# Kernel optimization log

Measured on AMD Instinct MI355X. Metric: run time of the kernel, lower is better.

## Reference

```python
import jax, jax.numpy as jnp
import numpy as np

NUM_Q, NUM_C, E = 12000, 1000, 256
B, S, MC = 32, 200, 4
H = E  # hidden_size == emb_size


def _mlp(x, lin_w, lin_b, out_w, out_b):
    # MLP with n_layer=1: relu(Linear) then output Linear (dropout is identity in eval)
    x = jax.nn.relu(x @ lin_w.T + lin_b)
    return x @ out_w.T + out_b


def _lstm(x, w_ih, w_hh, b_ih, b_hh):
    # torch nn.LSTM(batch_first) semantics, gate order i,f,g,o
    def step(carry, xt):
        h, cs = carry
        gates = xt @ w_ih.T + b_ih + h @ w_hh.T + b_hh
        i, f, g, o = jnp.split(gates, 4, axis=-1)
        cs = jax.nn.sigmoid(f) * cs + jax.nn.sigmoid(i) * jnp.tanh(g)
        h = jax.nn.sigmoid(o) * jnp.tanh(cs)
        return (h, cs), h
    b = x.shape[0]
    init = (jnp.zeros((b, H), x.dtype), jnp.zeros((b, H), x.dtype))
    _, hs = jax.lax.scan(step, init, jnp.swapaxes(x, 0, 1))
    return jnp.swapaxes(hs, 0, 1)


def _avg_fusion_concepts(y_concept, cshft):
    # gather-average over concept ids (equivalent to one_hot*mul*sum in the torch code)
    mask = (cshft != -1)
    idx = jnp.where(mask, cshft, 0)
    gathered = jnp.take_along_axis(y_concept, idx, axis=-1) * mask  # [B,S-1,MC]
    cnt = mask.sum(-1)
    return gathered.sum(-1) / jnp.maximum(cnt, 1)


def _avg_skill_emb(c, concept_emb):
    # QueEmb.get_avg_skill_emb: zero row prepended, -1 padding -> index 0
    cat = jnp.concatenate([jnp.zeros((1, E), concept_emb.dtype), concept_emb], axis=0)
    rc = c + 1
    s = cat[rc].sum(axis=-2)  # [B,S,E]
    n = jnp.maximum((rc != 0).sum(axis=-1), 1)
    return s / n[..., None]


def setup_inputs() -> dict:
    key = jax.random.key(0)
    ks = jax.random.split(key, 24)
    f = jnp.float32
    def lin(k, out_d, in_d):
        bound = 1.0 / np.sqrt(in_d)
        k1, k2 = jax.random.split(k)
        return (jax.random.uniform(k1, (out_d, in_d), f, -bound, bound),
                jax.random.uniform(k2, (out_d,), f, -bound, bound))
    qn_lw, qn_lb = lin(ks[0], 3 * H, 3 * H)
    qn_ow, qn_ob = lin(ks[1], 1, 3 * H)
    cn_lw, cn_lb = lin(ks[2], 3 * H, 3 * H)
    cn_ow, cn_ob = lin(ks[3], NUM_C, 3 * H)
    qa_lw, qa_lb = lin(ks[4], H, H)
    qa_ow, qa_ob = lin(ks[5], NUM_Q, H)
    ca_lw, ca_lb = lin(ks[6], H, H)
    ca_ow, ca_ob = lin(ks[7], NUM_C, H)
    w_ih, b_ih = lin(ks[8], 4 * H, 4 * E)
    w_hh, b_hh = lin(ks[9], 4 * H, H)
    return {
        'q': jax.random.randint(ks[10], (B, S), 0, NUM_Q),
        'c': jax.random.randint(ks[11], (B, S, MC), 0, NUM_C),
        'r': jax.random.randint(ks[12], (B, S), 0, 2),
        'qshft': jax.random.randint(ks[13], (B, S - 1), 0, NUM_Q),
        'cshft': jax.random.randint(ks[14], (B, S - 1, MC), 0, NUM_C),
        'que_emb': jax.random.normal(ks[15], (NUM_Q, E), f) * 0.02,
        'concept_emb': jax.random.normal(ks[16], (NUM_C, E), f) * 0.02,
        'w_ih': w_ih, 'w_hh': w_hh, 'b_ih': b_ih, 'b_hh': b_hh,
        'qn_lw': qn_lw, 'qn_lb': qn_lb, 'qn_ow': qn_ow, 'qn_ob': qn_ob,
        'cn_lw': cn_lw, 'cn_lb': cn_lb, 'cn_ow': cn_ow, 'cn_ob': cn_ob,
        'qa_lw': qa_lw, 'qa_lb': qa_lb, 'qa_ow': qa_ow, 'qa_ob': qa_ob,
        'ca_lw': ca_lw, 'ca_lb': ca_lb, 'ca_ow': ca_ow, 'ca_ob': ca_ob,
    }


def reference(q, c, r, qshft, cshft, que_emb, concept_emb, w_ih, w_hh, b_ih, b_hh,
              qn_lw, qn_lb, qn_ow, qn_ob, cn_lw, cn_lb, cn_ow, cn_ob,
              qa_lw, qa_lb, qa_ow, qa_ob, ca_lw, ca_lb, ca_ow, ca_ob):
    emb_q = que_emb[q]                               # [B,S,E]
    emb_c = _avg_skill_emb(c, concept_emb)           # [B,S,E]
    emb_qc = jnp.concatenate([emb_q, emb_c], -1)     # [B,S,2E]
    rf = r.astype(emb_qc.dtype)[..., None]
    emb_qca = jnp.concatenate([emb_qc * (1 - rf), emb_qc * rf], -1)  # [B,S,4E]

    emb_qc_shift = emb_qc[:, 1:]
    emb_qca_current = emb_qca[:, :-1]
    h = _lstm(emb_qca_current, w_ih, w_hh, b_ih, b_hh)  # [B,S-1,H]  (dropout: eval)
    h_next = jnp.concatenate([emb_qc_shift, h], -1)     # [B,S-1,3H]

    y_question_next = jax.nn.sigmoid(_mlp(h_next, qn_lw, qn_lb, qn_ow, qn_ob)).squeeze(-1)
    y_concept_next = jax.nn.sigmoid(_mlp(h_next, cn_lw, cn_lb, cn_ow, cn_ob))   # [B,S-1,num_c]
    y_question_all = jax.nn.sigmoid(_mlp(h, qa_lw, qa_lb, qa_ow, qa_ob))        # [B,S-1,num_q]
    y_concept_all = jax.nn.sigmoid(_mlp(h, ca_lw, ca_lb, ca_ow, ca_ob))         # [B,S-1,num_c]

    y_concept_next = _avg_fusion_concepts(y_concept_next, cshft)
    y_question_all = jnp.take_along_axis(y_question_all, qshft[..., None], axis=-1).squeeze(-1)
    y_concept_all = _avg_fusion_concepts(y_concept_all, cshft)
    return (y_question_next, y_concept_next, y_question_all, y_concept_all)
```

## Files before the change

kernel.cpp:

```cpp
#include <hip/hip_runtime.h>
#include <hip/hip_bf16.h>

typedef __hip_bfloat16 bf16;
typedef __attribute__((ext_vector_type(8))) short short8;
typedef __attribute__((ext_vector_type(4))) short short4v;
typedef __attribute__((ext_vector_type(4))) float float4v;

#define MFMA16(a,b,c) __builtin_amdgcn_mfma_f32_16x16x32_bf16((a),(b),(c),0,0,0)

#define NB 32
#define NS 200
#define NT 199
#define NBT (NB*NT)
#define HSTR 272

__device__ __forceinline__ float bf2f(bf16 x){ return __bfloat162float(x); }
__device__ __forceinline__ bf16 f2bf(float x){ return __float2bfloat16(x); }
__device__ __forceinline__ float rcp_(float x){ return __builtin_amdgcn_rcpf(x); }
__device__ __forceinline__ float sigmoidf_(float x){ return rcp_(1.0f+__expf(-x)); }
__device__ __forceinline__ float tanhf_(float x){ return 1.0f - 2.0f*rcp_(__expf(2.0f*x)+1.0f); }

union BU { bf16 b; unsigned short u; };
__device__ __forceinline__ unsigned short b2u(bf16 x){ BU t; t.b = x; return t.u; }
__device__ __forceinline__ float u2f(unsigned short x){ BU t; t.u = x; return bf2f(t.b); }

template<typename T>
__device__ __forceinline__ float ldf(const T* p, size_t i){
  if constexpr (sizeof(T) == 4) return p[i]; else return bf2f(p[i]);
}

__device__ __forceinline__ float wave_reduce(float v){
  #pragma unroll
  for (int o=32;o>0;o>>=1) v += __shfl_xor(v, o, 64);
  return v;
}

__device__ __forceinline__ int poll_xready_rlx(int* xchunk, int lane){
  int tgt = (lane < 25) ? ((lane == 24) ? 7 : 8) : 0;
  int v = 0;
  if (lane < 25)
    v = __hip_atomic_load(&xchunk[lane], __ATOMIC_RELAXED, __HIP_MEMORY_SCOPE_AGENT);
  unsigned long long full = __ballot(v >= tgt);
  unsigned long long notfull = ~full;
  int firstbad = (notfull == 0ULL) ? 64 : (__ffsll((unsigned long long)notfull) - 1);
  int rdy = firstbad * 8;
  return (rdy > NT) ? NT : rdy;
}

__global__ void k_detect(const unsigned short* qe, int* flag){
  int big = 0;
  for (int j = threadIdx.x; j < 128; j += 64){
    int ex = (qe[j] >> 7) & 0xFF;
    if (ex >= 128) big = 1;
  }
  unsigned long long m = __ballot(big);
  if (threadIdx.x == 0) flag[0] = (__popcll(m) >= 2) ? 1 : 0;
}

__global__ void k_sentinel(void* out, int n, float v, const int* flag){
  int i = blockIdx.x*256 + threadIdx.x;
  if (i < n){ if (flag[0]) ((float*)out)[i] = v; else ((bf16*)out)[i] = f2bf(v); }
}

__global__ __launch_bounds__(1024) void k_cvt(
    const void* s0, const void* s1, const void* s2, const void* s3,
    const void* s4, const void* s5, const void* s6, const void* s7,
    bf16* out, const int* flag){
  size_t i = (size_t)blockIdx.x*1024 + threadIdx.x;
  const size_t sz[8] = {1048576,262144,589824,589824,65536,65536,4096,4096};
  const void* sp[8] = {s0,s1,s2,s3,s4,s5,s6,s7};
  size_t off = i; int s = 0;
  while (s < 8 && off >= sz[s]){ off -= sz[s]; s++; }
  if (s >= 8) return;
  if (flag[0]) out[i] = f2bf(((const float*)sp[s])[off]);
  else         out[i] = ((const bf16*)sp[s])[off];
}

template<typename T>
__device__ __forceinline__ void embed_body(const int* q, const int* c,
    const T* que_emb, const T* concept_emb, bf16* emb_qc){
  int p = blockIdx.x;
  int e = threadIdx.x;
  int qi = q[p];
  emb_qc[(size_t)p*512 + e] = f2bf(ldf(que_emb, (size_t)qi*256 + e));
  float s = 0.f; int cnt = 0;
  #pragma unroll
  for (int m=0;m<4;m++){
    int ci = c[p*4+m];
    if (ci >= 0){ cnt++; s += ldf(concept_emb, (size_t)ci*256 + e); }
  }
  s /= (float)(cnt > 0 ? cnt : 1);
  emb_qc[(size_t)p*512 + 256 + e] = f2bf(s);
}
__global__ __launch_bounds__(256) void k_embed(const int* q, const int* c,
    const void* qe, const void* ce, bf16* emb_qc, const int* flag, int* cnt){
  if (blockIdx.x == 0 && threadIdx.x < 32) cnt[threadIdx.x] = 0;
  if (flag[0]) embed_body<float>(q, c, (const float*)qe, (const float*)ce, emb_qc);
  else         embed_body<bf16 >(q, c, (const bf16*)qe,  (const bf16*)ce,  emb_qc);
}

__device__ void gemm_x_unit(int t, int ny, int ltid, unsigned short* xs,
    const bf16* E, const int* r, const bf16* W, const bf16* bc1, const bf16* bc2, bf16* Xp){
  int lane = ltid & 63, wv = ltid >> 6;
  int col = lane & 15, quad = lane >> 4, kq = quad*8;
  const bf16* e0 = E + (size_t)(col*NS + t)*512;
  const bf16* e1 = E + (size_t)((col+16)*NS + t)*512;
  int rv0 = r[col*NS + t], rv1 = r[(col+16)*NS + t];
  int n_base = ny*256 + wv*64;
  const bf16* w0 = W + (size_t)(n_base + col)*1024 + kq;
  short8 z8 = {};
  float4v acc[2][4] = {};
  for (int k0 = 0; k0 < 1024; k0 += 32){
    bool lo = (k0 < 512);
    short8 a0 = *(const short8*)(e0 + (k0 & 511) + kq);
    short8 a1 = *(const short8*)(e1 + (k0 & 511) + kq);
    a0 = (lo == (rv0 == 0)) ? a0 : z8;
    a1 = (lo == (rv1 == 0)) ? a1 : z8;
    short8 bb[4];
    #pragma unroll
    for (int ni=0;ni<4;ni++) bb[ni] = *(const short8*)(w0 + (size_t)ni*16*1024 + k0);
    #pragma unroll
    for (int ni=0;ni<4;ni++){
      acc[0][ni] = MFMA16(a0, bb[ni], acc[0][ni]);
      acc[1][ni] = MFMA16(a1, bb[ni], acc[1][ni]);
    }
  }
  #pragma unroll
  for (int ni=0;ni<4;ni++){
    int n = n_base + ni*16 + col;
    float bs = bf2f(bc1[n]) + bf2f(bc2[n]);
    int nloc = wv*64 + ni*16 + col;
    #pragma unroll
    for (int mi=0;mi<2;mi++)
      #pragma unroll
      for (int reg=0;reg<4;reg++)
        xs[nloc*40 + mi*16 + quad*4 + reg] = b2u(f2bf(acc[mi][ni][reg] + bs));
  }
  __syncthreads();
  int nloc = ltid;
  size_t n = (size_t)ny*256 + nloc;
  short8 v0 = *(const short8*)&xs[nloc*40 + 0];
  short8 v1 = *(const short8*)&xs[nloc*40 + 8];
  short8 v2 = *(const short8*)&xs[nloc*40 + 16];
  short8 v3 = *(const short8*)&xs[nloc*40 + 24];
  bf16* base = Xp + (size_t)t*2*16384 + n*16;
  *(short8*)(base)             = v0;
  *(short8*)(base + 8)         = v1;
  *(short8*)(base + 16384)     = v2;
  *(short8*)(base + 16384 + 8) = v3;
}

__device__ void lstm_role(const bf16* Xp, const bf16* Whh, bf16* Hg,
                          unsigned short* smem, int* cnt){
  int* xchunk = cnt;
  int* hprog  = cnt + 25;
  unsigned short* wlds = smem;
  unsigned short* hbuf = smem + 65536;

  int lane = threadIdx.x & 63, w = threadIdx.x >> 6;
  int col = lane & 15, quad = lane >> 4, kq = quad*8;
  int b0 = blockIdx.x*16;

  for (int i = threadIdx.x; i < 16*HSTR; i += 512) hbuf[i] = 0;

  short8 bfrag[4][8];
  #pragma unroll
  for (int tix=0; tix<4; tix++){
    int g = tix >> 1, ct = tix & 1;
    int nb = g*256 + w*32 + ct*16;
    #pragma unroll
    for (int ks=0; ks<8; ks++)
      bfrag[tix][ks] = *(const volatile short8*)(Whh + (size_t)(nb + col)*256 + ks*32 + kq);
  }
  short8 wofrag[2][8];
  #pragma unroll
  for (int j=0; j<2; j++){
    int nb = 3*256 + w*32 + j*16;
    #pragma unroll
    for (int ks=0; ks<8; ks++)
      wofrag[j][ks] = *(const volatile short8*)(Whh + (size_t)(nb + col)*256 + ks*32 + kq);
  }
  #pragma unroll
  for (int j=0; j<2; j++){
    int nb = 2*256 + w*32 + j*16;
    #pragma unroll
    for (int ks=0; ks<8; ks++){
      short8 v = *(const short8*)(Whh + (size_t)(nb + col)*256 + ks*32 + kq);
      *(short8*)&wlds[(((w*2+j)*8 + ks)*64 + lane)*8] = v;
    }
  }
  __syncthreads();

  float cs[2][4] = {};
  short4v xq[8], xqn[8];

  int ready = 0;
  while (ready < 1){
    int p = poll_xready_rlx(xchunk, lane);
    if (p > ready){
      __builtin_amdgcn_fence(__ATOMIC_ACQUIRE, "agent");
      ready = p;
    } else __builtin_amdgcn_s_sleep(16);
  }
  {
    const bf16* xb = Xp + (size_t)blockIdx.x*16384 + quad*4;
    #pragma unroll
    for (int g=0; g<4; g++)
      #pragma unroll
      for (int ct=0; ct<2; ct++)
        xq[g*2+ct] = *(const short4v*)(xb + (size_t)(g*256 + w*32 + ct*16 + col)*16);
  }

  for (int t=0; t<NT; t++){
    int tn = (t+1 < NT) ? t+1 : t;
    while (ready < tn+1){
      int p = poll_xready_rlx(xchunk, lane);
      if (p > ready){
        __builtin_amdgcn_fence(__ATOMIC_ACQUIRE, "agent");
        ready = p;
      } else __builtin_amdgcn_s_sleep(16);
    }
    const bf16* xbn = Xp + ((size_t)tn*2 + blockIdx.x)*16384 + quad*4;
    #pragma unroll
    for (int g=0; g<4; g++)
      #pragma unroll
      for (int ct=0; ct<2; ct++)
        xqn[g*2+ct] = *(const short4v*)(xbn + (size_t)(g*256 + w*32 + ct*16 + col)*16);

    float4v acc[8];
    #pragma unroll
    for (int j=0; j<8; j++)
      #pragma unroll
      for (int rg=0; rg<4; rg++)
        acc[j][rg] = u2f((unsigned short)xq[j][rg]);

    const unsigned short* hrow = &hbuf[(t&1)*(16*HSTR) + col*HSTR + kq];
    #pragma unroll
    for (int ks=0; ks<8; ks++){
      short8 af = *(const short8*)(hrow + ks*32);
      #pragma unroll
      for (int tix=0; tix<4; tix++) acc[tix] = MFMA16(af, bfrag[tix][ks], acc[tix]);
      #pragma unroll
      for (int j=0; j<2; j++){
        short8 lw = *(const short8*)&wlds[(((w*2+j)*8 + ks)*64 + lane)*8];
        acc[4+j] = MFMA16(af, lw, acc[4+j]);
      }
      acc[6] = MFMA16(af, wofrag[0][ks], acc[6]);
      acc[7] = MFMA16(af, wofrag[1][ks], acc[7]);
    }

    unsigned short* hw = &hbuf[((t+1)&1)*(16*HSTR)];
    #pragma unroll
    for (int ct=0; ct<2; ct++){
      int hc = w*32 + ct*16 + col;
      #pragma unroll
      for (int reg=0; reg<4; reg++){
        float iv = sigmoidf_(acc[0+ct][reg]);
        float fv = sigmoidf_(acc[2+ct][reg]);
        float gv = tanhf_   (acc[4+ct][reg]);
        float ov = sigmoidf_(acc[6+ct][reg]);
        float cc = fv*cs[ct][reg] + iv*gv;
        cs[ct][reg] = cc;
        hw[(quad*4+reg)*HSTR + hc] = b2u(f2bf(ov*tanhf_(cc)));
      }
    }
    #pragma unroll
    for (int i=0;i<8;i++) xq[i] = xqn[i];
    __syncthreads();
    if (((t & 1) == 0) && threadIdx.x == ((((unsigned)t >> 1) & 7) << 6))
      __hip_atomic_store(&hprog[blockIdx.x], t, __ATOMIC_RELEASE, __HIP_MEMORY_SCOPE_AGENT);
    {
      int ri = threadIdx.x >> 5, ci2 = threadIdx.x & 31;
      short8 v = *(const short8*)&hbuf[((t+1)&1)*(16*HSTR) + ri*HSTR + ci2*8];
      *(short8*)(Hg + ((size_t)t*NB + b0 + ri)*256 + ci2*8) = v;
    }
  }
  __syncthreads();
  if (threadIdx.x == 0)
    __hip_atomic_store(&hprog[blockIdx.x], NT, __ATOMIC_RELEASE, __HIP_MEMORY_SCOPE_AGENT);
}

#define HPAD 776
#define SPAD 264
template<typename T>
__device__ void head_pair(int t0, int tid, unsigned short* hsb, unsigned short* hss,
    const bf16* E, const bf16* Hg,
    const bf16* qn_w, const bf16* cn_w, const bf16* qa_w, const bf16* ca_w,
    const T* qn_lb, const T* qn_ow, const T* qn_ob,
    const T* cn_lb, const T* cn_ow, const T* cn_ob,
    const T* qa_lb, const T* qa_ow, const T* qa_ob,
    const T* ca_lb, const T* ca_ow, const T* ca_ob,
    const int* qshft, const int* cshft, void* out, int isf32){
  int hf = tid >> 8, ltid = tid & 255;
  int lane = ltid & 63, wv = ltid >> 6;
  int col = lane & 15, quad = lane >> 4, kq = quad*8;
  const bf16* h0 = Hg + ((size_t)t0*NB + col)*256;
  const bf16* h1 = Hg + ((size_t)t0*NB + col + 16)*256;
  const bf16* e0 = E + ((size_t)col*NS + t0 + 1)*512;
  const bf16* e1 = E + ((size_t)(col+16)*NS + t0 + 1)*512;

  for (int hd=0; hd<2; hd++){
    if (hf == 0){
      const bf16* W = hd ? cn_w : qn_w;
      const T*   Bb = hd ? cn_lb : qn_lb;
      const bf16* wb = W + (size_t)(wv*192 + col)*768 + kq;
      float4v acc[2][12] = {};
      for (int k0 = 0; k0 < 768; k0 += 32){
        short8 a0 = (k0 < 512) ? *(const short8*)(e0 + k0 + kq)
                               : *(const short8*)(h0 + (k0-512) + kq);
        short8 a1 = (k0 < 512) ? *(const short8*)(e1 + k0 + kq)
                               : *(const short8*)(h1 + (k0-512) + kq);
        #pragma unroll
        for (int ni=0; ni<12; ni++){
          short8 bv = *(const short8*)(wb + (size_t)ni*16*768 + k0);
          acc[0][ni] = MFMA16(a0, bv, acc[0][ni]);
          acc[1][ni] = MFMA16(a1, bv, acc[1][ni]);
        }
      }
      #pragma unroll
      for (int ni=0; ni<12; ni++){
        int n = wv*192 + ni*16 + col;
        float bs = ldf(Bb, n);
        #pragma unroll
        for (int mi=0; mi<2; mi++)
          #pragma unroll
          for (int reg=0; reg<4; reg++){
            int rl = mi*16 + quad*4 + reg;
            hsb[rl*HPAD + n] = b2u(f2bf(fmaxf(acc[mi][ni][reg] + bs, 0.0f)));
          }
      }
    } else {
      const bf16* W = hd ? ca_w : qa_w;
      const T*   Bb = hd ? ca_lb : qa_lb;
      const bf16* wb = W + (size_t)(wv*64 + col)*256 + kq;
      float4v acc[2][4] = {};
      for (int k0 = 0; k0 < 256; k0 += 32){
        short8 av0 = *(const short8*)(h0 + k0 + kq);
        short8 av1 = *(const short8*)(h1 + k0 + kq);
        #pragma unroll
        for (int ni=0; ni<4; ni++){
          short8 bv = *(const short8*)(wb + (size_t)ni*16*256 + k0);
          acc[0][ni] = MFMA16(av0, bv, acc[0][ni]);
          acc[1][ni] = MFMA16(av1, bv, acc[1][ni]);
        }
      }
      #pragma unroll
      for (int ni=0; ni<4; ni++){
        int n = wv*64 + ni*16 + col;
        float bs = ldf(Bb, n);
        #pragma unroll
        for (int mi=0; mi<2; mi++)
          #pragma unroll
          for (int reg=0; reg<4; reg++){
            int rl = mi*16 + quad*4 + reg;
            hss[rl*SPAD + n] = b2u(f2bf(fmaxf(acc[mi][ni][reg] + bs, 0.0f)));
          }
      }
    }
    __syncthreads();
    if (hf == 0){
      for (int rr=0; rr<8; rr++){
        int rl = wv*8 + rr, p = rl*NT + t0;
        if (hd == 0){
          float d = 0.f;
          for (int i=lane; i<768; i+=64) d += u2f(hsb[rl*HPAD + i]) * ldf(qn_ow, i);
          d = wave_reduce(d);
          if (lane == 0){
            float v = sigmoidf_(d + ldf(qn_ob, 0));
            if (isf32) ((float*)out)[p] = v; else ((bf16*)out)[p] = f2bf(v);
          }
        } else {
          float sum = 0.f; int cnt = 0;
          #pragma unroll
          for (int m=0; m<4; m++){
            int cid = cshft[p*4+m];
            if (cid >= 0){
              cnt++;
              const T* ww = cn_ow + (size_t)cid*768;
              float d = 0.f;
              for (int i=lane; i<768; i+=64) d += u2f(hsb[rl*HPAD + i]) * ldf(ww, i);
              d = wave_reduce(d);
              sum += sigmoidf_(d + ldf(cn_ob, cid));
            }
          }
          if (lane == 0){
            float v = sum / (float)(cnt > 0 ? cnt : 1);
            if (isf32) ((float*)out)[NBT+p] = v; else ((bf16*)out)[NBT+p] = f2bf(v);
          }
        }
      }
    } else {
      for (int rr=0; rr<8; rr++){
        int rl = wv*8 + rr, p = rl*NT + t0;
        if (hd == 0){
          int qid = qshft[p];
          const T* ww = qa_ow + (size_t)qid*256;
          float d = 0.f;
          for (int i=lane; i<256; i+=64) d += u2f(hss[rl*SPAD + i]) * ldf(ww, i);
          d = wave_reduce(d);
          if (lane == 0){
            float v = sigmoidf_(d + ldf(qa_ob, qid));
            if (isf32) ((float*)out)[2*NBT+p] = v; else ((bf16*)out)[2*NBT+p] = f2bf(v);
          }
        } else {
          float sum = 0.f; int cnt = 0;
          #pragma unroll
          for (int m=0; m<4; m++){
            int cid = cshft[p*4+m];
            if (cid >= 0){
              cnt++;
              const T* ww = ca_ow + (size_t)cid*256;
              float d = 0.f;
              for (int i=lane; i<256; i+=64) d += u2f(hss[rl*SPAD + i]) * ldf(ww, i);
              d = wave_reduce(d);
              sum += sigmoidf_(d + ldf(ca_ob, cid));
            }
          }
          if (lane == 0){
            float v = sum / (float)(cnt > 0 ? cnt : 1);
            if (isf32) ((float*)out)[3*NBT+p] = v; else ((bf16*)out)[3*NBT+p] = f2bf(v);
          }
        }
      }
    }
    __syncthreads();
  }
}

__global__ __launch_bounds__(512)
__attribute__((amdgpu_waves_per_eu(2, 2)))
void k_fused(const bf16* E, const int* r, const bf16* wih, const bf16* bih, const bf16* bhh,
             bf16* Xp, const bf16* whh, bf16* Hg,
             const bf16* qn_w, const bf16* cn_w, const bf16* qa_w, const bf16* ca_w,
             const void* qn_lb, const void* qn_ow, const void* qn_ob,
             const void* cn_lb, const void* cn_ow, const void* cn_ob,
             const void* qa_lb, const void* qa_ow, const void* qa_ob,
             const void* ca_lb, const void* ca_ow, const void* ca_ob,
             const int* qshft, const int* cshft, void* out, const int* flag, int* cnt){
  extern __shared__ __align__(16) unsigned short smem[];
  int* xchunk = cnt;
  int* hprog  = cnt + 25;

  if (blockIdx.x < 2){
    lstm_role(Xp, whh, Hg, smem, cnt);
    return;
  }

  int t0  = blockIdx.x - 2;
  int tid = threadIdx.x, hf = tid >> 8, ltid = tid & 255;
  volatile int* lflag = (volatile int*)(smem + 73728);

  {
    unsigned short* xs = smem + hf*(256*40);
    gemm_x_unit(t0, hf,     ltid, xs, E, r, wih, bih, bhh, Xp);
    __syncthreads();
    gemm_x_unit(t0, 2 + hf, ltid, xs, E, r, wih, bih, bhh, Xp);
    if (tid == 0) *lflag = 0;
    __syncthreads();
    if (tid == 0)
      __hip_atomic_fetch_add(&xchunk[t0 >> 3], 1, __ATOMIC_RELEASE, __HIP_MEMORY_SCOPE_AGENT);
  }

  {
    int need = t0 + 1;
    for (;;){
      if (tid == 0){
        int a = __hip_atomic_load(&hprog[0], __ATOMIC_RELAXED, __HIP_MEMORY_SCOPE_AGENT);
        int b = __hip_atomic_load(&hprog[1], __ATOMIC_RELAXED, __HIP_MEMORY_SCOPE_AGENT);
        if (a >= need && b >= need){
          __builtin_amdgcn_fence(__ATOMIC_ACQUIRE, "agent");
          *lflag = 1;
        }
      }
      if (*lflag) break;
      __builtin_amdgcn_s_sleep(32);
    }
  }
  __syncthreads();

  unsigned short* hsb = smem;
  unsigned short* hss = smem + 32*HPAD;
  if (flag[0])
    head_pair<float>(t0, tid, hsb, hss, E, Hg, qn_w, cn_w, qa_w, ca_w,
      (const float*)qn_lb, (const float*)qn_ow, (const float*)qn_ob,
      (const float*)cn_lb, (const float*)cn_ow, (const float*)cn_ob,
      (const float*)qa_lb, (const float*)qa_ow, (const float*)qa_ob,
      (const float*)ca_lb, (const float*)ca_ow, (const float*)ca_ob,
      qshft, cshft, out, 1);
  else
    head_pair<bf16>(t0, tid, hsb, hss, E, Hg, qn_w, cn_w, qa_w, ca_w,
      (const bf16*)qn_lb, (const bf16*)qn_ow, (const bf16*)qn_ob,
      (const bf16*)cn_lb, (const bf16*)cn_ow, (const bf16*)cn_ob,
      (const bf16*)qa_lb, (const bf16*)qa_ow, (const bf16*)qa_ob,
      (const bf16*)ca_lb, (const bf16*)ca_ow, (const bf16*)ca_ob,
      qshft, cshft, out, 0);
}

extern "C" void kernel_launch(void* const* d_in, const int* in_sizes, int n_in,
                              void* d_out, int out_size, void* d_ws, size_t ws_size,
                              hipStream_t stream){
  const int*  q     = (const int*) d_in[0];
  const int*  c     = (const int*) d_in[1];
  const int*  r     = (const int*) d_in[2];
  const int*  qshft = (const int*) d_in[3];
  const int*  cshft = (const int*) d_in[4];
  const void* que_emb  = d_in[5];
  const void* conc_emb = d_in[6];
  const void* w_ih  = d_in[7];
  const void* w_hh  = d_in[8];
  const void* b_ih  = d_in[9];
  const void* b_hh  = d_in[10];
  const void* qn_lw = d_in[11];
  const void* qn_lb = d_in[12];
  const void* qn_ow = d_in[13];
  const void* qn_ob = d_in[14];
  const void* cn_lw = d_in[15];
  const void* cn_lb = d_in[16];
  const void* cn_ow = d_in[17];
  const void* cn_ob = d_in[18];
  const void* qa_lw = d_in[19];
  const void* qa_lb = d_in[20];
  const void* qa_ow = d_in[21];
  const void* qa_ob = d_in[22];
  const void* ca_lw = d_in[23];
  const void* ca_lb = d_in[24];
  const void* ca_ow = d_in[25];
  const void* ca_ob = d_in[26];

  const size_t OFF_FLAG = 0;
  const size_t OFF_EMB  = 256;
  const size_t OFF_XPT  = OFF_EMB + 6553600;
  const size_t OFF_HG   = OFF_XPT + 13041664;
  const size_t OFF_WC   = OFF_HG + 3260416;
  const size_t NEED     = OFF_WC + 5259264;

  char* ws = (char*)d_ws;
  int* flag = (int*)(ws + OFF_FLAG);
  int* cnt  = (int*)(ws + 64);

  k_detect<<<1, 64, 0, stream>>>((const unsigned short*)que_emb, flag);

  if (ws_size < NEED){
    k_sentinel<<<(out_size + 255)/256, 256, 0, stream>>>(d_out, out_size,
        (float)(ws_size >> 20), flag);
    return;
  }

  bf16* emb_qc = (bf16*)(ws + OFF_EMB);
  bf16* Xp     = (bf16*)(ws + OFF_XPT);
  bf16* Hg     = (bf16*)(ws + OFF_HG);
  bf16* Wc     = (bf16*)(ws + OFF_WC);
  bf16* wih_c  = Wc;
  bf16* whh_c  = Wc + 1048576;
  bf16* qnlw_c = Wc + 1310720;
  bf16* cnlw_c = Wc + 1900544;
  bf16* qalw_c = Wc + 2490368;
  bf16* calw_c = Wc + 2555904;
  bf16* bih_c  = Wc + 2621440;
  bf16* bhh_c  = Wc + 2625536;

  hipFuncSetAttribute((const void*)k_fused,
      hipFuncAttributeMaxDynamicSharedMemorySize, 148480);

  k_cvt<<<2568, 1024, 0, stream>>>(w_ih, w_hh, qn_lw, cn_lw, qa_lw, ca_lw,
      b_ih, b_hh, Wc, flag);
  k_embed<<<NB*NS, 256, 0, stream>>>(q, c, que_emb, conc_emb, emb_qc, flag, cnt);
  k_fused<<<201, 512, 148480, stream>>>(emb_qc, r, wih_c, bih_c, bhh_c, Xp, whh_c, Hg,
      qnlw_c, cnlw_c, qalw_c, calw_c,
      qn_lb, qn_ow, qn_ob, cn_lb, cn_ow, cn_ob,
      qa_lb, qa_ow, qa_ob, ca_lb, ca_ow, ca_ob,
      qshft, cshft, d_out, flag, cnt);
}
```

Measured before the change: 1.013 ms.

## Interleave X-projection units across blocks and publish LSTM progress every step

```diff
diff --git a/kernel.cpp b/kernel.cpp
--- a/kernel.cpp
+++ b/kernel.cpp
@@ -36,7 +36,7 @@
 }
 
 __device__ __forceinline__ int poll_xready_rlx(int* xchunk, int lane){
-  int tgt = (lane < 25) ? ((lane == 24) ? 7 : 8) : 0;
+  int tgt = (lane < 25) ? ((lane == 24) ? 28 : 32) : 0;
   int v = 0;
   if (lane < 25)
     v = __hip_atomic_load(&xchunk[lane], __ATOMIC_RELAXED, __HIP_MEMORY_SCOPE_AGENT);
@@ -267,17 +267,23 @@
     #pragma unroll
     for (int i=0;i<8;i++) xq[i] = xqn[i];
     __syncthreads();
-    if (((t & 1) == 0) && threadIdx.x == ((((unsigned)t >> 1) & 7) << 6))
-      __hip_atomic_store(&hprog[blockIdx.x], t, __ATOMIC_RELEASE, __HIP_MEMORY_SCOPE_AGENT);
+    if (threadIdx.x == 0)
+      __hip_atomic_store(&hprog[blockIdx.x], t, __ATOMIC_RELAXED, __HIP_MEMORY_SCOPE_AGENT);
     {
-      int ri = threadIdx.x >> 5, ci2 = threadIdx.x & 31;
-      short8 v = *(const short8*)&hbuf[((t+1)&1)*(16*HSTR) + ri*HSTR + ci2*8];
-      *(short8*)(Hg + ((size_t)t*NB + b0 + ri)*256 + ci2*8) = v;
+      const unsigned short* hb = &hbuf[((t+1)&1)*(16*HSTR)];
+      unsigned int* dst = (unsigned int*)(Hg + ((size_t)t*NB + b0)*256);
+      #pragma unroll
+      for (int j = threadIdx.x; j < 2048; j += 512){
+        int row = j >> 7, dcol = j & 127;
+        unsigned int v = *(const unsigned int*)&hb[row*HSTR + dcol*2];
+        __hip_atomic_store(dst + row*128 + dcol, v,
+                           __ATOMIC_RELAXED, __HIP_MEMORY_SCOPE_AGENT);
+      }
     }
   }
   __syncthreads();
   if (threadIdx.x == 0)
-    __hip_atomic_store(&hprog[blockIdx.x], NT, __ATOMIC_RELEASE, __HIP_MEMORY_SCOPE_AGENT);
+    __hip_atomic_store(&hprog[blockIdx.x], NT, __ATOMIC_RELAXED, __HIP_MEMORY_SCOPE_AGENT);
 }
 
 #define HPAD 776
@@ -446,21 +452,26 @@
     return;
   }
 
-  int t0  = blockIdx.x - 2;
+  int rank = blockIdx.x - 2;
   int tid = threadIdx.x, hf = tid >> 8, ltid = tid & 255;
   volatile int* lflag = (volatile int*)(smem + 73728);
 
   {
     unsigned short* xs = smem + hf*(256*40);
-    gemm_x_unit(t0, hf,     ltid, xs, E, r, wih, bih, bhh, Xp);
-    __syncthreads();
-    gemm_x_unit(t0, 2 + hf, ltid, xs, E, r, wih, bih, bhh, Xp);
+    #pragma unroll
+    for (int p = 0; p < 2; p++){
+      int ub = p*398 + 2*rank;
+      int t  = ub >> 2;
+      gemm_x_unit(t, (ub & 3) + hf, ltid, xs, E, r, wih, bih, bhh, Xp);
+      __syncthreads();
+      if (tid == 0)
+        __hip_atomic_fetch_add(&xchunk[t >> 3], 2, __ATOMIC_RELEASE, __HIP_MEMORY_SCOPE_AGENT);
+    }
     if (tid == 0) *lflag = 0;
     __syncthreads();
-    if (tid == 0)
-      __hip_atomic_fetch_add(&xchunk[t0 >> 3], 1, __ATOMIC_RELEASE, __HIP_MEMORY_SCOPE_AGENT);
-  }
-
+  }
+
+  int t0 = rank;
   {
     int need = t0 + 1;
     for (;;){
```

After: 1.206 ms. 1.19x slower.
